# Kernel tuning notes

Hardware: AMD Instinct MI355X
Metric: run time of the kernel (lower is better)

## Reference

```python
import math
import jax, jax.numpy as jnp
import numpy as np

C1, D, NUM_HEADS, K_CH = 150, 32, 4, 10
GLOBAL_TOPK_RATIO = 0.08


def _pos2d(h, w, dim):
    d2 = dim // 2
    div = jnp.exp(jnp.arange(0, d2, 2, dtype=jnp.float32) * (-(math.log(10000.0) / d2)))
    def axis_pe(n):
        ang = jnp.arange(n, dtype=jnp.float32)[:, None] * div[None, :]
        pe = jnp.zeros((n, d2), dtype=jnp.float32)
        pe = pe.at[:, 0::2].set(jnp.sin(ang))
        pe = pe.at[:, 1::2].set(jnp.cos(ang))
        return pe
    pe_y = axis_pe(h)  # [h, d2]
    pe_x = axis_pe(w)  # [w, d2]
    return jnp.concatenate([
        jnp.broadcast_to(pe_y[:, None, :], (h, w, d2)),
        jnp.broadcast_to(pe_x[None, :, :], (h, w, d2)),
    ], axis=-1)  # [h, w, dim]


def setup_inputs() -> dict:
    key = jax.random.key(0)
    ks = jax.random.split(key, 7)
    B = 1024
    return {
        "x": jax.random.uniform(ks[0], (B, 1, 28, 28), dtype=jnp.float32),
        "conv1_w": jax.random.normal(ks[1], (C1, 1, 9, 9), dtype=jnp.float32) * 0.05,
        "channel_embed": jax.random.normal(ks[2], (C1, D), dtype=jnp.float32) * 0.02,
        "in_proj_w": jax.random.normal(ks[3], (3 * D, D), dtype=jnp.float32) * (1.0 / math.sqrt(D)),
        "in_proj_b": jnp.zeros((3 * D,), dtype=jnp.float32),
        "out_proj_w": jax.random.normal(ks[4], (D, D), dtype=jnp.float32) * (1.0 / math.sqrt(D)),
        "out_proj_b": jnp.zeros((D,), dtype=jnp.float32),
    }


def reference(x, conv1_w, channel_embed, in_proj_w, in_proj_b, out_proj_w, out_proj_b):
    # conv1 + relu: [B,1,28,28] -> [B,150,14,14]
    A = jax.nn.relu(jax.lax.conv_general_dilated(
        x, conv1_w, window_strides=(2, 2), padding=((4, 4), (4, 4)),
        dimension_numbers=("NCHW", "OIHW", "NCHW")))
    B, C, H, W = A.shape
    total = C * H * W
    k_global = max(1, int(math.ceil(GLOBAL_TOPK_RATIO * total)))
    A_flat = A.reshape(B, -1)
    # global kthvalue threshold: k_global-th largest per sample
    thresh = jax.lax.top_k(A_flat, k_global)[0][:, -1:]
    A_global = (A_flat * (A_flat >= thresh)).reshape(B, C, H, W)
    # per-location channel top-k + scatter
    v = jnp.transpose(A_global, (0, 2, 3, 1))  # [B,H,W,C]
    topv, topi = jax.lax.top_k(v, K_CH)        # [B,H,W,k]
    N = B * H * W
    logits = jnp.zeros((N, C), v.dtype).at[
        jnp.arange(N)[:, None], topi.reshape(N, K_CH)
    ].set(topv.reshape(N, K_CH)).reshape(v.shape)
    # normalize by per-sample global max (guard zero)
    flat_logits = logits.reshape(B, -1)
    gmax = jnp.max(flat_logits, axis=1, keepdims=True)
    normed = jnp.where(gmax == 0, 0.0, flat_logits / jnp.where(gmax == 0, 1.0, gmax))
    sparse_weights = normed.reshape(logits.shape)  # [B,H,W,C]
    # channel embedding + 2D sinusoidal PE
    loc_emb = jnp.einsum("bhwc,cd->bhwd", sparse_weights, channel_embed)
    loc_emb = loc_emb + _pos2d(H, W, D)[None]
    seq = loc_emb.reshape(B, H * W, D)
    # 1-layer MHA (self-attention, batch_first)
    qkv = seq @ in_proj_w.T + in_proj_b  # [B,S,3D]
    q, k, vv = jnp.split(qkv, 3, axis=-1)
    hd = D // NUM_HEADS
    def heads(t):
        return jnp.transpose(t.reshape(B, H * W, NUM_HEADS, hd), (0, 2, 1, 3))
    q, k, vv = heads(q), heads(k), heads(vv)
    attn = jax.nn.softmax(jnp.einsum("bnsd,bntd->bnst", q, k) / math.sqrt(hd), axis=-1)
    ctx = jnp.einsum("bnst,bntd->bnsd", attn, vv)
    ctx = jnp.transpose(ctx, (0, 2, 1, 3)).reshape(B, H * W, D)
    attn_out = ctx @ out_proj_w.T + out_proj_b  # [B, 196, 32]
    return attn_out
```

## Files before the change

### kernel.cpp

```cpp
#include <hip/hip_runtime.h>
#include <math.h>

#define NC1 150
#define HW 196
#define NB 1024
#define DD 32
#define NHD 4
#define HDIM 8
#define KG 2352
#define KCH 10
#define CAP 48
#define CVS 49
#define CES 36
#define KVS 20

#define UNI_F 17552
#define XT_OFF 0
#define WT_OFF 8232
#define CV_OFF 0
#define CC_OFF 9604
#define CNT_OFF 11956
#define CE_OFF 12152

__global__ void pos2d_kernel(float* __restrict__ pos) {
  int i = blockIdx.x * 256 + threadIdx.x;
  if (i >= HW * DD) return;
  int s = i >> 5, d = i & 31;
  int h = s / 14, w = s % 14;
  int p = (d < 16) ? h : w;
  int dd = (d < 16) ? d : d - 16;
  int j = dd >> 1;
  float dv = expf(-(logf(10000.0f) / 16.0f) * (float)(2 * j));
  float ang = (float)p * dv;
  pos[i] = (dd & 1) ? cosf(ang) : sinf(ang);
}

__global__ void prep_kernel(const float* __restrict__ cw, float* __restrict__ wtg) {
  int i = blockIdx.x * 256 + threadIdx.x;
  if (i >= 84 * 152) return;
  int k = i / 152, c = i - k * 152;
  wtg[i] = (k < 81 && c < NC1) ? cw[c * 81 + k] : 0.f;
}

__global__ __launch_bounds__(1024, 8) void fused_kernel(const float* __restrict__ x,
                                                        const float* __restrict__ wtg,
                                                        const float* __restrict__ CE,
                                                        const float* __restrict__ pos,
                                                        float* __restrict__ seqo) {
  __shared__ alignas(16) float uni[UNI_F];
  __shared__ alignas(16) float xs[784];
  __shared__ unsigned hist[2048];
  __shared__ unsigned wsum[4];
  __shared__ unsigned s_prefix, s_krem, s_max;

  int b = blockIdx.x, tid = threadIdx.x;
  int lane = tid & 63, wid = tid >> 6;

  if (tid < 196) ((float4*)xs)[tid] = ((const float4*)(x + (size_t)b * 784))[tid];
  if (tid == 0) { s_prefix = 0u; s_krem = KG; s_max = 0u; }
  __syncthreads();

  int cg = tid / 49;
  int g  = tid - cg * 49;
  bool act = (tid < 931);
  float acc[4][8];
#pragma unroll
  for (int i = 0; i < 4; ++i)
#pragma unroll
    for (int j = 0; j < 8; ++j) acc[i][j] = 0.f;

  float* XT = uni + XT_OFF;
  float* WT = uni + WT_OFF;

  for (int kb = 0; kb < 84; kb += 42) {
    for (int i = tid; i < 42 * 196; i += 1024) {
      int kk = i / 196, s = i - kk * 196;
      int k = kb + kk;
      float v = 0.f;
      if (k < 81) {
        int ki = k / 9, kj = k - ki * 9;
        int h = s / 14, w = s - h * 14;
        int r = 2 * h - 4 + ki, c = 2 * w - 4 + kj;
        if (r >= 0 && r < 28 && c >= 0 && c < 28) v = xs[r * 28 + c];
      }
      XT[i] = v;
    }
    for (int i = tid; i < (42 * 152) / 4; i += 1024)
      ((float4*)WT)[i] = ((const float4*)(wtg + kb * 152))[i];
    __syncthreads();
    if (act) {
      const float* xtp = XT + 4 * g;
      const float* wtp = WT + 8 * cg;
#pragma unroll 7
      for (int kk = 0; kk < 42; ++kk) {
        float4 xv = *(const float4*)(xtp + kk * 196);
        float4 w0 = *(const float4*)(wtp + kk * 152);
        float4 w1 = *(const float4*)(wtp + kk * 152 + 4);
        float xa[4] = {xv.x, xv.y, xv.z, xv.w};
        float wa[8] = {w0.x, w0.y, w0.z, w0.w, w1.x, w1.y, w1.z, w1.w};
#pragma unroll
        for (int i = 0; i < 4; ++i)
#pragma unroll
          for (int j = 0; j < 8; ++j) acc[i][j] += xa[i] * wa[j];
      }
    }
    __syncthreads();
  }

#pragma unroll
  for (int i = 0; i < 4; ++i)
#pragma unroll
    for (int j = 0; j < 8; ++j) acc[i][j] = fmaxf(acc[i][j], 0.f);

  for (int pass = 0; pass < 3; ++pass) {
    hist[tid] = 0u; hist[tid + 1024] = 0u;
    __syncthreads();
    int shift = (pass == 0) ? 21 : (pass == 1 ? 10 : 0);
    int bits = (pass == 2) ? 10 : 11;
    unsigned mask = (1u << bits) - 1u;
    unsigned pfx = s_prefix;
    unsigned krem = s_krem;
    int hishift = shift + bits;
    if (pass == 0) {
      unsigned mymax = 0u;
#pragma unroll
      for (int i = 0; i < 4; ++i)
#pragma unroll
        for (int j = 0; j < 8; ++j) {
          unsigned u = __float_as_uint(acc[i][j]);
          mymax = max(mymax, u);
          if (u) atomicAdd(&hist[u >> 21], 1u);
        }
#pragma unroll
      for (int st = 32; st >= 1; st >>= 1)
        mymax = max(mymax, (unsigned)__shfl_xor((int)mymax, st));
      if (lane == 0) atomicMax(&s_max, mymax);
    } else {
#pragma unroll
      for (int i = 0; i < 4; ++i)
#pragma unroll
        for (int j = 0; j < 8; ++j) {
          unsigned u = __float_as_uint(acc[i][j]);
          if (u && (u >> hishift) == pfx) atomicAdd(&hist[(u >> shift) & mask], 1u);
        }
    }
    __syncthreads();
    int segsz = (1 << bits) >> 8;
    unsigned segv = 0u, sufv = 0u;
    if (tid < 256) {
      for (int j = 0; j < segsz; ++j) segv += hist[tid * segsz + j];
      sufv = segv;
#pragma unroll
      for (int st = 1; st < 64; st <<= 1) {
        unsigned o = (unsigned)__shfl_down((int)sufv, st);
        if (lane + st < 64) sufv += o;
      }
      if (lane == 0) wsum[wid] = sufv;
    }
    __syncthreads();
    if (tid < 256) {
      unsigned tail = 0u;
      for (int ww = wid + 1; ww < 4; ++ww) tail += wsum[ww];
      sufv += tail;
      unsigned above = sufv - segv;
      if (above < krem && sufv >= krem) {
        unsigned cum = above;
        int dsel = tid * segsz;
        for (int d2 = segsz - 1; d2 >= 0; --d2) {
          int dd = tid * segsz + d2;
          if (cum + hist[dd] >= krem) { dsel = dd; break; }
          cum += hist[dd];
        }
        s_prefix = (pfx << bits) | (unsigned)dsel;
        s_krem = krem - cum;
      }
    }
    __syncthreads();
  }

  float* candV = uni + CV_OFF;
  unsigned char* candC = (unsigned char*)(uni + CC_OFF);
  unsigned* cnt = (unsigned*)(uni + CNT_OFF);
  if (tid < 196) cnt[tid] = 0u;
  __syncthreads();
  float T = __uint_as_float(s_prefix);
  if (act) {
#pragma unroll
    for (int i = 0; i < 4; ++i) {
      int loc = 4 * g + i;
#pragma unroll
      for (int j = 0; j < 8; ++j) {
        float v = acc[i][j];
        if (v >= T && v > 0.f) {
          unsigned slot = atomicAdd(&cnt[loc], 1u);
          if (slot < CAP) {
            candV[loc * CVS + slot] = v;
            candC[loc * CAP + slot] = (unsigned char)(8 * cg + j);
          }
        }
      }
    }
  }
  __syncthreads();

  float* CEs = uni + CE_OFF;
  if (tid >= 196) {
    for (int i = tid - 196; i < NC1 * 32; i += 1024 - 196) {
      int c = i >> 5, e = i & 31;
      CEs[c * CES + e] = CE[i];
    }
  }
  float tv[KCH]; int tc[KCH];
  if (tid < 196) {
    int loc = tid;
    unsigned n = cnt[loc]; if (n > CAP) n = CAP;
#pragma unroll
    for (int k = 0; k < KCH; ++k) { tv[k] = 0.f; tc[k] = 0; }
    for (unsigned jj = 0; jj < n; ++jj) {
      float v = candV[loc * CVS + jj];
      int c = candC[loc * CAP + jj];
      if (v > tv[KCH - 1] || (v == tv[KCH - 1] && c < tc[KCH - 1])) {
        float iv = v; int ic = c;
#pragma unroll
        for (int j = 0; j < KCH; ++j) {
          bool gt = (iv > tv[j]) || (iv == tv[j] && ic < tc[j]);
          float nv = gt ? iv : tv[j]; int nc = gt ? ic : tc[j];
          float ov = gt ? tv[j] : iv; int oc = gt ? tc[j] : ic;
          tv[j] = nv; tc[j] = nc; iv = ov; ic = oc;
        }
      }
    }
  }
  __syncthreads();

  if (tid < 196) {
    float gm = __uint_as_float(s_max);
    float gi = (gm == 0.0f) ? 0.0f : 1.0f / gm;
    float acc2[32];
#pragma unroll
    for (int e = 0; e < 32; ++e) acc2[e] = 0.f;
#pragma unroll
    for (int k = 0; k < KCH; ++k) {
      float v = tv[k];
      const float4* cr = (const float4*)(CEs + tc[k] * CES);
#pragma unroll
      for (int e4 = 0; e4 < 8; ++e4) {
        float4 cv = cr[e4];
        acc2[e4 * 4 + 0] += v * cv.x;
        acc2[e4 * 4 + 1] += v * cv.y;
        acc2[e4 * 4 + 2] += v * cv.z;
        acc2[e4 * 4 + 3] += v * cv.w;
      }
    }
    float* op = seqo + ((size_t)b * HW + tid) * DD;
    const float* pr = pos + tid * DD;
#pragma unroll
    for (int e4 = 0; e4 < 8; ++e4) {
      float4 pv = ((const float4*)pr)[e4];
      float4 o;
      o.x = acc2[e4 * 4 + 0] * gi + pv.x;
      o.y = acc2[e4 * 4 + 1] * gi + pv.y;
      o.z = acc2[e4 * 4 + 2] * gi + pv.z;
      o.w = acc2[e4 * 4 + 3] * gi + pv.w;
      ((float4*)op)[e4] = o;
    }
  }
}

__global__ __launch_bounds__(832, 3) void attn_kernel(const float* __restrict__ seq,
                                                      const float* __restrict__ Wqkv,
                                                      const float* __restrict__ bqkv,
                                                      float* __restrict__ ctxo) {
  __shared__ alignas(16) float kvs[NHD * HW * KVS];
  __shared__ alignas(16) float swq[96 * DD];
  __shared__ float sbq[96];
  __shared__ unsigned s_kk[NHD];

  int b = blockIdx.x, tid = threadIdx.x;
  int h = tid / HW;
  int s = tid - h * HW;
  bool act = (tid < NHD * HW);

  float xr[32];
  if (act) {
    const float* row = seq + ((size_t)b * HW + s) * DD;
#pragma unroll
    for (int e = 0; e < 8; ++e) {
      float4 f = ((const float4*)row)[e];
      xr[e * 4 + 0] = f.x; xr[e * 4 + 1] = f.y; xr[e * 4 + 2] = f.z; xr[e * 4 + 3] = f.w;
    }
  }
  for (int i = tid; i < (96 * DD) / 4; i += 832)
    ((float4*)swq)[i] = ((const float4*)Wqkv)[i];
  if (tid < 96) sbq[tid] = bqkv[tid];
  if (tid < NHD) s_kk[tid] = 0u;
  __syncthreads();

  float q[8]; float qq = 0.f;
  if (act) {
    float* kvrow = kvs + ((size_t)h * HW + s) * KVS;
    {
      float ka[8]; float kk = 0.f;
#pragma unroll
      for (int d = 0; d < 8; ++d) {
        const float* wr = swq + (32 + h * HDIM + d) * DD;
        float acc = sbq[32 + h * HDIM + d];
#pragma unroll
        for (int e = 0; e < DD; e += 4) {
          float4 wv = *(const float4*)(wr + e);
          acc += xr[e + 0] * wv.x + xr[e + 1] * wv.y + xr[e + 2] * wv.z + xr[e + 3] * wv.w;
        }
        ka[d] = acc; kk += acc * acc;
      }
      float4 k0 = {ka[0], ka[1], ka[2], ka[3]}, k1 = {ka[4], ka[5], ka[6], ka[7]};
      ((float4*)kvrow)[0] = k0; ((float4*)kvrow)[1] = k1;
      atomicMax(&s_kk[h], __float_as_uint(kk));
    }
    {
      float va[8];
#pragma unroll
      for (int d = 0; d < 8; ++d) {
        const float* wr = swq + (64 + h * HDIM + d) * DD;
        float acc = sbq[64 + h * HDIM + d];
#pragma unroll
        for (int e = 0; e < DD; e += 4) {
          float4 wv = *(const float4*)(wr + e);
          acc += xr[e + 0] * wv.x + xr[e + 1] * wv.y + xr[e + 2] * wv.z + xr[e + 3] * wv.w;
        }
        va[d] = acc;
      }
      float4 v0 = {va[0], va[1], va[2], va[3]}, v1 = {va[4], va[5], va[6], va[7]};
      ((float4*)kvrow)[2] = v0; ((float4*)kvrow)[3] = v1;
    }
#pragma unroll
    for (int d = 0; d < 8; ++d) {
      const float* wr = swq + (h * HDIM + d) * DD;
      float acc = sbq[h * HDIM + d];
#pragma unroll
      for (int e = 0; e < DD; e += 4) {
        float4 wv = *(const float4*)(wr + e);
        acc += xr[e + 0] * wv.x + xr[e + 1] * wv.y + xr[e + 2] * wv.z + xr[e + 3] * wv.w;
      }
      q[d] = acc; qq += acc * acc;
    }
  }
  __syncthreads();
  if (!act) return;

  const float scale = 0.3535533905932738f;
  float kkmax = __uint_as_float(s_kk[h]);
  float negM = -sqrtf(qq * kkmax) * scale;
  float l = 0.f;
  float c0 = 0.f, c1 = 0.f, c2 = 0.f, c3 = 0.f, c4 = 0.f, c5 = 0.f, c6 = 0.f, c7 = 0.f;
  const float4* kp = (const float4*)(kvs + (size_t)h * HW * KVS);
#pragma unroll 4
  for (int t = 0; t < HW; ++t) {
    float4 k0 = kp[0], k1 = kp[1], v0 = kp[2], v1 = kp[3];
    kp += 5;
    float sc = q[0] * k0.x;
    sc = fmaf(q[1], k0.y, sc); sc = fmaf(q[2], k0.z, sc); sc = fmaf(q[3], k0.w, sc);
    sc = fmaf(q[4], k1.x, sc); sc = fmaf(q[5], k1.y, sc); sc = fmaf(q[6], k1.z, sc);
    sc = fmaf(q[7], k1.w, sc);
    float p = __expf(fmaf(sc, scale, negM));
    l += p;
    c0 = fmaf(p, v0.x, c0); c1 = fmaf(p, v0.y, c1); c2 = fmaf(p, v0.z, c2);
    c3 = fmaf(p, v0.w, c3); c4 = fmaf(p, v1.x, c4); c5 = fmaf(p, v1.y, c5);
    c6 = fmaf(p, v1.z, c6); c7 = fmaf(p, v1.w, c7);
  }
  float inv = 1.0f / l;
  float* op = ctxo + ((size_t)b * HW + s) * DD + h * HDIM;
  float4 o0, o1;
  o0.x = c0 * inv; o0.y = c1 * inv; o0.z = c2 * inv; o0.w = c3 * inv;
  o1.x = c4 * inv; o1.y = c5 * inv; o1.z = c6 * inv; o1.w = c7 * inv;
  ((float4*)op)[0] = o0; ((float4*)op)[1] = o1;
}

__global__ __launch_bounds__(256) void outproj_kernel(const float* __restrict__ ctx,
                                                      const float* __restrict__ Wo,
                                                      const float* __restrict__ bo,
                                                      float* __restrict__ out) {
  __shared__ float sw[32 * 32];
  __shared__ float sb2[32];
  int tid = threadIdx.x;
  for (int i = tid; i < 1024; i += 256) sw[i] = Wo[i];
  if (tid < 32) sb2[tid] = bo[tid];
  __syncthreads();
  size_t row = (size_t)blockIdx.x * 256 + tid;
  const float* cr = ctx + row * 32;
  float xr[32];
#pragma unroll
  for (int e = 0; e < 8; ++e) {
    float4 f = ((const float4*)cr)[e];
    xr[e * 4 + 0] = f.x; xr[e * 4 + 1] = f.y; xr[e * 4 + 2] = f.z; xr[e * 4 + 3] = f.w;
  }
  float* op = out + row * 32;
#pragma unroll
  for (int d4 = 0; d4 < 8; ++d4) {
    float4 o;
    float* oo = (float*)&o;
#pragma unroll
    for (int q = 0; q < 4; ++q) {
      int d = d4 * 4 + q;
      float acc = sb2[d];
      const float* wr = sw + d * 32;
#pragma unroll
      for (int e = 0; e < 32; e += 4) {
        float4 wv = *(const float4*)(wr + e);
        acc += xr[e + 0] * wv.x + xr[e + 1] * wv.y + xr[e + 2] * wv.z + xr[e + 3] * wv.w;
      }
      oo[q] = acc;
    }
    ((float4*)op)[d4] = o;
  }
}

extern "C" void kernel_launch(void* const* d_in, const int* in_sizes, int n_in,
                              void* d_out, int out_size, void* d_ws, size_t ws_size,
                              hipStream_t stream) {
  const float* x  = (const float*)d_in[0];
  const float* cw = (const float*)d_in[1];
  const float* ce = (const float*)d_in[2];
  const float* wq = (const float*)d_in[3];
  const float* bq = (const float*)d_in[4];
  const float* wo = (const float*)d_in[5];
  const float* bo = (const float*)d_in[6];
  float* out = (float*)d_out;
  float* ws  = (float*)d_ws;

  float* ctx = ws;
  float* pos = ws + (size_t)NB * HW * DD;
  float* wtg = pos + HW * DD;

  prep_kernel<<<(84 * 152 + 255) / 256, 256, 0, stream>>>(cw, wtg);
  pos2d_kernel<<<(HW * DD + 255) / 256, 256, 0, stream>>>(pos);
  fused_kernel<<<NB, 1024, 0, stream>>>(x, wtg, ce, pos, out);
  attn_kernel<<<NB, 832, 0, stream>>>(out, wq, bq, ctx);
  outproj_kernel<<<(NB * HW * DD) / (256 * 32), 256, 0, stream>>>(ctx, wo, bo, out);
}
```

Baseline: 394.9 us.

## Fuse output projection into attention kernel and read weights directly from global

```diff
diff --git a/kernel.cpp b/kernel.cpp
--- a/kernel.cpp
+++ b/kernel.cpp
@@ -13,6 +13,7 @@
 #define CVS 49
 #define CES 36
 #define KVS 20
+#define CXS 36
 
 #define UNI_F 17552
 #define XT_OFF 0
@@ -270,16 +271,17 @@
 __global__ __launch_bounds__(832, 3) void attn_kernel(const float* __restrict__ seq,
                                                       const float* __restrict__ Wqkv,
                                                       const float* __restrict__ bqkv,
-                                                      float* __restrict__ ctxo) {
+                                                      const float* __restrict__ Wo,
+                                                      const float* __restrict__ bo,
+                                                      float* __restrict__ outp) {
   __shared__ alignas(16) float kvs[NHD * HW * KVS];
-  __shared__ alignas(16) float swq[96 * DD];
-  __shared__ float sbq[96];
   __shared__ unsigned s_kk[NHD];
 
   int b = blockIdx.x, tid = threadIdx.x;
   int h = tid / HW;
   int s = tid - h * HW;
   bool act = (tid < NHD * HW);
+  if (tid < NHD) s_kk[tid] = 0u;
 
   float xr[32];
   if (act) {
@@ -290,21 +292,17 @@
       xr[e * 4 + 0] = f.x; xr[e * 4 + 1] = f.y; xr[e * 4 + 2] = f.z; xr[e * 4 + 3] = f.w;
     }
   }
-  for (int i = tid; i < (96 * DD) / 4; i += 832)
-    ((float4*)swq)[i] = ((const float4*)Wqkv)[i];
-  if (tid < 96) sbq[tid] = bqkv[tid];
-  if (tid < NHD) s_kk[tid] = 0u;
   __syncthreads();
 
   float q[8]; float qq = 0.f;
   if (act) {
-    float* kvrow = kvs + ((size_t)h * HW + s) * KVS;
+    float* kvrow = kvs + (h * HW + s) * KVS;
     {
       float ka[8]; float kk = 0.f;
 #pragma unroll
       for (int d = 0; d < 8; ++d) {
-        const float* wr = swq + (32 + h * HDIM + d) * DD;
-        float acc = sbq[32 + h * HDIM + d];
+        const float* wr = Wqkv + (32 + h * HDIM + d) * DD;
+        float acc = bqkv[32 + h * HDIM + d];
 #pragma unroll
         for (int e = 0; e < DD; e += 4) {
           float4 wv = *(const float4*)(wr + e);
@@ -320,8 +318,8 @@
       float va[8];
 #pragma unroll
       for (int d = 0; d < 8; ++d) {
-        const float* wr = swq + (64 + h * HDIM + d) * DD;
-        float acc = sbq[64 + h * HDIM + d];
+        const float* wr = Wqkv + (64 + h * HDIM + d) * DD;
+        float acc = bqkv[64 + h * HDIM + d];
 #pragma unroll
         for (int e = 0; e < DD; e += 4) {
           float4 wv = *(const float4*)(wr + e);
@@ -334,8 +332,8 @@
     }
 #pragma unroll
     for (int d = 0; d < 8; ++d) {
-      const float* wr = swq + (h * HDIM + d) * DD;
-      float acc = sbq[h * HDIM + d];
+      const float* wr = Wqkv + (h * HDIM + d) * DD;
+      float acc = bqkv[h * HDIM + d];
 #pragma unroll
       for (int e = 0; e < DD; e += 4) {
         float4 wv = *(const float4*)(wr + e);
@@ -345,72 +343,67 @@
     }
   }
   __syncthreads();
-  if (!act) return;
-
-  const float scale = 0.3535533905932738f;
-  float kkmax = __uint_as_float(s_kk[h]);
-  float negM = -sqrtf(qq * kkmax) * scale;
+
+  float c0 = 0.f, c1 = 0.f, c2 = 0.f, c3 = 0.f, c4 = 0.f, c5 = 0.f, c6 = 0.f, c7 = 0.f;
   float l = 0.f;
-  float c0 = 0.f, c1 = 0.f, c2 = 0.f, c3 = 0.f, c4 = 0.f, c5 = 0.f, c6 = 0.f, c7 = 0.f;
-  const float4* kp = (const float4*)(kvs + (size_t)h * HW * KVS);
+  if (act) {
+    const float scaleL = 0.3535533905932738f * 1.4426950408889634f;
+    float kkmax = __uint_as_float(s_kk[h]);
+    float negML = -sqrtf(qq * kkmax) * scaleL;
+    const float4* kp = (const float4*)(kvs + (h * HW) * KVS);
+    const float4* kpr = kp + s * 0;
 #pragma unroll 4
-  for (int t = 0; t < HW; ++t) {
-    float4 k0 = kp[0], k1 = kp[1], v0 = kp[2], v1 = kp[3];
-    kp += 5;
-    float sc = q[0] * k0.x;
-    sc = fmaf(q[1], k0.y, sc); sc = fmaf(q[2], k0.z, sc); sc = fmaf(q[3], k0.w, sc);
-    sc = fmaf(q[4], k1.x, sc); sc = fmaf(q[5], k1.y, sc); sc = fmaf(q[6], k1.z, sc);
-    sc = fmaf(q[7], k1.w, sc);
-    float p = __expf(fmaf(sc, scale, negM));
-    l += p;
-    c0 = fmaf(p, v0.x, c0); c1 = fmaf(p, v0.y, c1); c2 = fmaf(p, v0.z, c2);
-    c3 = fmaf(p, v0.w, c3); c4 = fmaf(p, v1.x, c4); c5 = fmaf(p, v1.y, c5);
-    c6 = fmaf(p, v1.z, c6); c7 = fmaf(p, v1.w, c7);
-  }
-  float inv = 1.0f / l;
-  float* op = ctxo + ((size_t)b * HW + s) * DD + h * HDIM;
-  float4 o0, o1;
-  o0.x = c0 * inv; o0.y = c1 * inv; o0.z = c2 * inv; o0.w = c3 * inv;
-  o1.x = c4 * inv; o1.y = c5 * inv; o1.z = c6 * inv; o1.w = c7 * inv;
-  ((float4*)op)[0] = o0; ((float4*)op)[1] = o1;
-}
-
-__global__ __launch_bounds__(256) void outproj_kernel(const float* __restrict__ ctx,
-                                                      const float* __restrict__ Wo,
-                                                      const float* __restrict__ bo,
-                                                      float* __restrict__ out) {
-  __shared__ float sw[32 * 32];
-  __shared__ float sb2[32];
-  int tid = threadIdx.x;
-  for (int i = tid; i < 1024; i += 256) sw[i] = Wo[i];
-  if (tid < 32) sb2[tid] = bo[tid];
-  __syncthreads();
-  size_t row = (size_t)blockIdx.x * 256 + tid;
-  const float* cr = ctx + row * 32;
-  float xr[32];
-#pragma unroll
-  for (int e = 0; e < 8; ++e) {
-    float4 f = ((const float4*)cr)[e];
-    xr[e * 4 + 0] = f.x; xr[e * 4 + 1] = f.y; xr[e * 4 + 2] = f.z; xr[e * 4 + 3] = f.w;
-  }
-  float* op = out + row * 32;
-#pragma unroll
-  for (int d4 = 0; d4 < 8; ++d4) {
-    float4 o;
-    float* oo = (float*)&o;
-#pragma unroll
-    for (int q = 0; q < 4; ++q) {
-      int d = d4 * 4 + q;
-      float acc = sb2[d];
-      const float* wr = sw + d * 32;
-#pragma unroll
-      for (int e = 0; e < 32; e += 4) {
+    for (int t = 0; t < HW; ++t) {
+      float4 k0 = kp[0], k1 = kp[1], v0 = kp[2], v1 = kp[3];
+      kp += 5;
+      float sc = q[0] * k0.x;
+      sc = fmaf(q[1], k0.y, sc); sc = fmaf(q[2], k0.z, sc); sc = fmaf(q[3], k0.w, sc);
+      sc = fmaf(q[4], k1.x, sc); sc = fmaf(q[5], k1.y, sc); sc = fmaf(q[6], k1.z, sc);
+      sc = fmaf(q[7], k1.w, sc);
+      float p = exp2f(fmaf(sc, scaleL, negML));
+      l += p;
+      c0 = fmaf(p, v0.x, c0); c1 = fmaf(p, v0.y, c1); c2 = fmaf(p, v0.z, c2);
+      c3 = fmaf(p, v0.w, c3); c4 = fmaf(p, v1.x, c4); c5 = fmaf(p, v1.y, c5);
+      c6 = fmaf(p, v1.z, c6); c7 = fmaf(p, v1.w, c7);
+    }
+    (void)kpr;
+  }
+  __syncthreads();
+
+  float* cx = kvs;
+  if (act) {
+    float inv = 1.0f / l;
+    float4 o0, o1;
+    o0.x = c0 * inv; o0.y = c1 * inv; o0.z = c2 * inv; o0.w = c3 * inv;
+    o1.x = c4 * inv; o1.y = c5 * inv; o1.z = c6 * inv; o1.w = c7 * inv;
+    float* cr = cx + s * CXS + h * HDIM;
+    ((float4*)cr)[0] = o0; ((float4*)cr)[1] = o1;
+  }
+  __syncthreads();
+
+  if (act) {
+    float xr2[32];
+    const float* crow = cx + s * CXS;
+#pragma unroll
+    for (int e = 0; e < 8; ++e) {
+      float4 f = ((const float4*)crow)[e];
+      xr2[e * 4 + 0] = f.x; xr2[e * 4 + 1] = f.y; xr2[e * 4 + 2] = f.z; xr2[e * 4 + 3] = f.w;
+    }
+    float oa[8];
+#pragma unroll
+    for (int d = 0; d < 8; ++d) {
+      const float* wr = Wo + (h * HDIM + d) * DD;
+      float acc = bo[h * HDIM + d];
+#pragma unroll
+      for (int e = 0; e < DD; e += 4) {
         float4 wv = *(const float4*)(wr + e);
-        acc += xr[e + 0] * wv.x + xr[e + 1] * wv.y + xr[e + 2] * wv.z + xr[e + 3] * wv.w;
-      }
-      oo[q] = acc;
-    }
-    ((float4*)op)[d4] = o;
+        acc += xr2[e + 0] * wv.x + xr2[e + 1] * wv.y + xr2[e + 2] * wv.z + xr2[e + 3] * wv.w;
+      }
+      oa[d] = acc;
+    }
+    float* op = outp + ((size_t)b * HW + s) * DD + h * HDIM;
+    float4 o0 = {oa[0], oa[1], oa[2], oa[3]}, o1 = {oa[4], oa[5], oa[6], oa[7]};
+    ((float4*)op)[0] = o0; ((float4*)op)[1] = o1;
   }
 }
 
@@ -427,13 +420,11 @@
   float* out = (float*)d_out;
   float* ws  = (float*)d_ws;
 
-  float* ctx = ws;
   float* pos = ws + (size_t)NB * HW * DD;
   float* wtg = pos + HW * DD;
 
   prep_kernel<<<(84 * 152 + 255) / 256, 256, 0, stream>>>(cw, wtg);
   pos2d_kernel<<<(HW * DD + 255) / 256, 256, 0, stream>>>(pos);
   fused_kernel<<<NB, 1024, 0, stream>>>(x, wtg, ce, pos, out);
-  attn_kernel<<<NB, 832, 0, stream>>>(out, wq, bq, ctx);
-  outproj_kernel<<<(NB * HW * DD) / (256 * 32), 256, 0, stream>>>(ctx, wo, bo, out);
+  attn_kernel<<<NB, 832, 0, stream>>>(out, wq, bq, wo, bo, out);
 }
```

After: 523.4 us. 32.5% more time.

## Split attention blocks per head pair and merge prep kernels

Applied to the files above, without the earlier changes.

```diff
diff --git a/kernel.cpp b/kernel.cpp
--- a/kernel.cpp
+++ b/kernel.cpp
@@ -22,24 +22,25 @@
 #define CNT_OFF 11956
 #define CE_OFF 12152
 
-__global__ void pos2d_kernel(float* __restrict__ pos) {
+__global__ void prep2_kernel(const float* __restrict__ cw, float* __restrict__ wtg,
+                             float* __restrict__ pos) {
   int i = blockIdx.x * 256 + threadIdx.x;
-  if (i >= HW * DD) return;
-  int s = i >> 5, d = i & 31;
-  int h = s / 14, w = s % 14;
-  int p = (d < 16) ? h : w;
-  int dd = (d < 16) ? d : d - 16;
-  int j = dd >> 1;
-  float dv = expf(-(logf(10000.0f) / 16.0f) * (float)(2 * j));
-  float ang = (float)p * dv;
-  pos[i] = (dd & 1) ? cosf(ang) : sinf(ang);
-}
-
-__global__ void prep_kernel(const float* __restrict__ cw, float* __restrict__ wtg) {
-  int i = blockIdx.x * 256 + threadIdx.x;
-  if (i >= 84 * 152) return;
-  int k = i / 152, c = i - k * 152;
-  wtg[i] = (k < 81 && c < NC1) ? cw[c * 81 + k] : 0.f;
+  if (i < HW * DD) {
+    int s = i >> 5, d = i & 31;
+    int h = s / 14, w = s % 14;
+    int p = (d < 16) ? h : w;
+    int dd = (d < 16) ? d : d - 16;
+    int j = dd >> 1;
+    float dv = expf(-(logf(10000.0f) / 16.0f) * (float)(2 * j));
+    float ang = (float)p * dv;
+    pos[i] = (dd & 1) ? cosf(ang) : sinf(ang);
+    return;
+  }
+  int j = i - HW * DD;
+  if (j < 84 * 152) {
+    int k = j / 152, c = j - k * 152;
+    wtg[j] = (k < 81 && c < NC1) ? cw[c * 81 + k] : 0.f;
+  }
 }
 
 __global__ __launch_bounds__(1024, 8) void fused_kernel(const float* __restrict__ x,
@@ -267,19 +268,21 @@
   }
 }
 
-__global__ __launch_bounds__(832, 3) void attn_kernel(const float* __restrict__ seq,
+__global__ __launch_bounds__(448, 4) void attn_kernel(const float* __restrict__ seq,
                                                       const float* __restrict__ Wqkv,
                                                       const float* __restrict__ bqkv,
                                                       float* __restrict__ ctxo) {
-  __shared__ alignas(16) float kvs[NHD * HW * KVS];
-  __shared__ alignas(16) float swq[96 * DD];
-  __shared__ float sbq[96];
-  __shared__ unsigned s_kk[NHD];
-
-  int b = blockIdx.x, tid = threadIdx.x;
+  __shared__ alignas(16) float kvs[2 * HW * KVS];
+  __shared__ alignas(16) float swq[48 * DD];
+  __shared__ float sbq[48];
+  __shared__ unsigned s_kk[2];
+
+  int blk = blockIdx.x;
+  int b = blk >> 1, hp = blk & 1;
+  int tid = threadIdx.x;
   int h = tid / HW;
   int s = tid - h * HW;
-  bool act = (tid < NHD * HW);
+  bool act = (tid < 2 * HW);
 
   float xr[32];
   if (act) {
@@ -290,17 +293,40 @@
       xr[e * 4 + 0] = f.x; xr[e * 4 + 1] = f.y; xr[e * 4 + 2] = f.z; xr[e * 4 + 3] = f.w;
     }
   }
-  for (int i = tid; i < (96 * DD) / 4; i += 832)
-    ((float4*)swq)[i] = ((const float4*)Wqkv)[i];
-  if (tid < 96) sbq[tid] = bqkv[tid];
-  if (tid < NHD) s_kk[tid] = 0u;
+  for (int i = tid; i < 48 * 8; i += 448) {
+    int r = i >> 3, c4 = i & 7;
+    int seg = r >> 4, lr = r & 15;
+    ((float4*)swq)[i] = ((const float4*)(Wqkv + (seg * 32 + hp * 16 + lr) * DD))[c4];
+  }
+  if (tid < 48) {
+    int seg = tid >> 4, lr = tid & 15;
+    sbq[tid] = bqkv[seg * 32 + hp * 16 + lr];
+  }
+  if (tid < 2) s_kk[tid] = 0u;
   __syncthreads();
 
   float q[8]; float qq = 0.f;
   if (act) {
-    float* kvrow = kvs + ((size_t)h * HW + s) * KVS;
+    float* kvrow = kvs + (h * HW + s) * KVS;
     {
       float ka[8]; float kk = 0.f;
+#pragma unroll
+      for (int d = 0; d < 8; ++d) {
+        const float* wr = swq + (16 + h * HDIM + d) * DD;
+        float acc = sbq[16 + h * HDIM + d];
+#pragma unroll
+        for (int e = 0; e < DD; e += 4) {
+          float4 wv = *(const float4*)(wr + e);
+          acc += xr[e + 0] * wv.x + xr[e + 1] * wv.y + xr[e + 2] * wv.z + xr[e + 3] * wv.w;
+        }
+        ka[d] = acc; kk += acc * acc;
+      }
+      float4 k0 = {ka[0], ka[1], ka[2], ka[3]}, k1 = {ka[4], ka[5], ka[6], ka[7]};
+      ((float4*)kvrow)[0] = k0; ((float4*)kvrow)[1] = k1;
+      atomicMax(&s_kk[h], __float_as_uint(kk));
+    }
+    {
+      float va[8];
 #pragma unroll
       for (int d = 0; d < 8; ++d) {
         const float* wr = swq + (32 + h * HDIM + d) * DD;
@@ -310,23 +336,6 @@
           float4 wv = *(const float4*)(wr + e);
           acc += xr[e + 0] * wv.x + xr[e + 1] * wv.y + xr[e + 2] * wv.z + xr[e + 3] * wv.w;
         }
-        ka[d] = acc; kk += acc * acc;
-      }
-      float4 k0 = {ka[0], ka[1], ka[2], ka[3]}, k1 = {ka[4], ka[5], ka[6], ka[7]};
-      ((float4*)kvrow)[0] = k0; ((float4*)kvrow)[1] = k1;
-      atomicMax(&s_kk[h], __float_as_uint(kk));
-    }
-    {
-      float va[8];
-#pragma unroll
-      for (int d = 0; d < 8; ++d) {
-        const float* wr = swq + (64 + h * HDIM + d) * DD;
-        float acc = sbq[64 + h * HDIM + d];
-#pragma unroll
-        for (int e = 0; e < DD; e += 4) {
-          float4 wv = *(const float4*)(wr + e);
-          acc += xr[e + 0] * wv.x + xr[e + 1] * wv.y + xr[e + 2] * wv.z + xr[e + 3] * wv.w;
-        }
         va[d] = acc;
       }
       float4 v0 = {va[0], va[1], va[2], va[3]}, v1 = {va[4], va[5], va[6], va[7]};
@@ -347,12 +356,12 @@
   __syncthreads();
   if (!act) return;
 
-  const float scale = 0.3535533905932738f;
+  const float scaleL = 0.3535533905932738f * 1.4426950408889634f;
   float kkmax = __uint_as_float(s_kk[h]);
-  float negM = -sqrtf(qq * kkmax) * scale;
+  float negML = -sqrtf(qq * kkmax) * scaleL;
   float l = 0.f;
   float c0 = 0.f, c1 = 0.f, c2 = 0.f, c3 = 0.f, c4 = 0.f, c5 = 0.f, c6 = 0.f, c7 = 0.f;
-  const float4* kp = (const float4*)(kvs + (size_t)h * HW * KVS);
+  const float4* kp = (const float4*)(kvs + (h * HW) * KVS);
 #pragma unroll 4
   for (int t = 0; t < HW; ++t) {
     float4 k0 = kp[0], k1 = kp[1], v0 = kp[2], v1 = kp[3];
@@ -361,14 +370,14 @@
     sc = fmaf(q[1], k0.y, sc); sc = fmaf(q[2], k0.z, sc); sc = fmaf(q[3], k0.w, sc);
     sc = fmaf(q[4], k1.x, sc); sc = fmaf(q[5], k1.y, sc); sc = fmaf(q[6], k1.z, sc);
     sc = fmaf(q[7], k1.w, sc);
-    float p = __expf(fmaf(sc, scale, negM));
+    float p = exp2f(fmaf(sc, scaleL, negML));
     l += p;
     c0 = fmaf(p, v0.x, c0); c1 = fmaf(p, v0.y, c1); c2 = fmaf(p, v0.z, c2);
     c3 = fmaf(p, v0.w, c3); c4 = fmaf(p, v1.x, c4); c5 = fmaf(p, v1.y, c5);
     c6 = fmaf(p, v1.z, c6); c7 = fmaf(p, v1.w, c7);
   }
   float inv = 1.0f / l;
-  float* op = ctxo + ((size_t)b * HW + s) * DD + h * HDIM;
+  float* op = ctxo + ((size_t)b * HW + s) * DD + (hp * 2 + h) * HDIM;
   float4 o0, o1;
   o0.x = c0 * inv; o0.y = c1 * inv; o0.z = c2 * inv; o0.w = c3 * inv;
   o1.x = c4 * inv; o1.y = c5 * inv; o1.z = c6 * inv; o1.w = c7 * inv;
@@ -431,9 +440,8 @@
   float* pos = ws + (size_t)NB * HW * DD;
   float* wtg = pos + HW * DD;
 
-  prep_kernel<<<(84 * 152 + 255) / 256, 256, 0, stream>>>(cw, wtg);
-  pos2d_kernel<<<(HW * DD + 255) / 256, 256, 0, stream>>>(pos);
+  prep2_kernel<<<(HW * DD + 84 * 152 + 255) / 256, 256, 0, stream>>>(cw, wtg, pos);
   fused_kernel<<<NB, 1024, 0, stream>>>(x, wtg, ce, pos, out);
-  attn_kernel<<<NB, 832, 0, stream>>>(out, wq, bq, ctx);
+  attn_kernel<<<NB * 2, 448, 0, stream>>>(out, wq, bq, ctx);
   outproj_kernel<<<(NB * HW * DD) / (256 * 32), 256, 0, stream>>>(ctx, wo, bo, out);
 }
```

Measured after the change: 419.6 us. +6.3%, slower.
